# Optimization experiments

Measured on AMD Instinct MI355X. Metric: run time of the kernel, lower is better.

The kernel has to match this reference:

```python
import jax, jax.numpy as jnp
import numpy as np

N = 50000      # nodes
E = 100000     # edges
F_NODE = 128
F_EDGE = 16
H = 64         # hidden_dim
OUT = 32
STEPS = 3
G = 64         # num_graphs (static; batch.max()+1 in torch)


def setup_inputs() -> dict:
    key = jax.random.key(0)
    ks = jax.random.split(key, 20)

    def lin(k, fin, fout):
        s = 1.0 / np.sqrt(fin)
        return jax.random.uniform(k, (fin, fout), jnp.float32, -s, s)

    def bias(k, fin, fout):
        s = 1.0 / np.sqrt(fin)
        return jax.random.uniform(k, (fout,), jnp.float32, -s, s)

    inp = {
        'x': jax.random.normal(ks[0], (N, F_NODE), jnp.float32),
        'edge_index': jax.random.randint(ks[1], (2, E), 0, N),
        'edge_attr': jax.random.normal(ks[2], (E, F_EDGE), jnp.float32),
        'batch': jnp.sort(jax.random.randint(ks[3], (N,), 0, G)),
        # node encoder
        'W_enc': lin(ks[4], F_NODE, H), 'b_enc': bias(ks[5], F_NODE, H),
        # edge_nn: Linear(F_EDGE,H) -> ReLU -> Linear(H, H*H)
        'W_e1': lin(ks[6], F_EDGE, H), 'b_e1': bias(ks[7], F_EDGE, H),
        'W_e2': lin(ks[8], H, H * H), 'b_e2': bias(ks[9], H, H * H),
        # GRUCell (torch layout: [3H, H])
        'W_ih': jax.random.uniform(ks[10], (3 * H, H), jnp.float32, -1/np.sqrt(H), 1/np.sqrt(H)),
        'W_hh': jax.random.uniform(ks[11], (3 * H, H), jnp.float32, -1/np.sqrt(H), 1/np.sqrt(H)),
        'b_ih': jax.random.uniform(ks[12], (3 * H,), jnp.float32, -1/np.sqrt(H), 1/np.sqrt(H)),
        'b_hh': jax.random.uniform(ks[13], (3 * H,), jnp.float32, -1/np.sqrt(H), 1/np.sqrt(H)),
        # readout MLP: Linear(H,H) -> ReLU -> Linear(H,OUT)
        'W_r1': lin(ks[14], H, H), 'b_r1': bias(ks[15], H, H),
        'W_r2': lin(ks[16], H, OUT), 'b_r2': bias(ks[17], H, OUT),
    }
    return inp


def gru_cell(m, h, W_ih, W_hh, b_ih, b_hh):
    gi = m @ W_ih.T + b_ih   # [N, 3H]
    gh = h @ W_hh.T + b_hh
    i_r, i_z, i_n = jnp.split(gi, 3, axis=-1)
    h_r, h_z, h_n = jnp.split(gh, 3, axis=-1)
    r = jax.nn.sigmoid(i_r + h_r)
    z = jax.nn.sigmoid(i_z + h_z)
    n = jnp.tanh(i_n + r * h_n)
    return (1.0 - z) * n + z * h


def reference(x, edge_index, edge_attr, batch, W_enc, b_enc, W_e1, b_e1,
              W_e2, b_e2, W_ih, W_hh, b_ih, b_hh, W_r1, b_r1, W_r2, b_r2):
    h = x @ W_enc + b_enc                                   # [N, H]
    src, dst = edge_index[0], edge_index[1]
    # edge-conditioned weight matrices (loop-invariant; compute once)
    ew = (jax.nn.relu(edge_attr @ W_e1 + b_e1) @ W_e2 + b_e2).reshape(E, H, H)
    for _ in range(STEPS):
        msg = jnp.einsum('eij,ej->ei', ew, h[src])          # per-edge matvec
        m_agg = jax.ops.segment_sum(msg, dst, num_segments=N)
        h = gru_cell(m_agg, h, W_ih, W_hh, b_ih, b_hh)
    g = jax.ops.segment_sum(h, batch, num_segments=G)       # sum readout
    return jax.nn.relu(g @ W_r1 + b_r1) @ W_r2 + b_r2
```

## Files before the change

### kernel.cpp

```cpp
#include <hip/hip_runtime.h>
#include <hip/hip_bf16.h>
#include <math.h>

#define NN 50000
#define NE 100000
#define FN 128
#define FE 16
#define HD 64
#define OUTD 32
#define NG 64
#define ZK 65

typedef unsigned int uint;
typedef unsigned short ushort;
typedef __attribute__((ext_vector_type(8))) short short8;
typedef __attribute__((ext_vector_type(16))) float f32x16;

static __device__ __forceinline__ float bfbits2f(uint u) {
    return __builtin_bit_cast(float, u << 16);
}
static __device__ __forceinline__ uint packbf(float f0, float f1) {
    return __builtin_amdgcn_perm(__builtin_bit_cast(uint, f1),
                                 __builtin_bit_cast(uint, f0), 0x07060302u);
}
static __device__ __forceinline__ ushort f2bf(float f) {
    uint u = __builtin_bit_cast(uint, f);
    u = (u + 0x7FFFu + ((u >> 16) & 1u)) >> 16;
    return (ushort)u;
}
static __device__ __forceinline__ uint pack2rne(float f0, float f1) {
    return (uint)f2bf(f0) | ((uint)f2bf(f1) << 16);
}
static __device__ __forceinline__ float fsigmoid(float x) {
    return 1.f / (1.f + __expf(-x));
}
static __device__ __forceinline__ float ftanh(float x) {
    float t = __expf(2.f * x);
    return 1.f - 2.f / (t + 1.f);
}

#define PREP_S0 (ZK * 4096)
#define PREP_S1 (256 * 128)
__global__ void k_prep(const float* __restrict__ W_e2, const float* __restrict__ b_e2,
                       const float* __restrict__ W_ih, const float* __restrict__ W_hh,
                       ushort* __restrict__ Wtb, ushort* __restrict__ Bg) {
    int idx = blockIdx.x * 256 + threadIdx.x;
    if (idx < PREP_S0) {
        int k0 = idx >> 12, r = idx & 4095;
        int i = r >> 6, j = r & 63;
        float v = (k0 < 64) ? W_e2[k0 * 4096 + i * 64 + j] : b_e2[i * 64 + j];
        Wtb[idx] = f2bf(v);
        return;
    }
    idx -= PREP_S0;
    if (idx < PREP_S1) {
        int n = idx >> 7, k = idx & 127;
        int g = n >> 6, i = n & 63;
        float v = 0.f;
        if (g == 0)      v = (k < 64) ? W_ih[i * 64 + k]         : W_hh[i * 64 + (k - 64)];
        else if (g == 1) v = (k < 64) ? W_ih[(64 + i) * 64 + k]  : W_hh[(64 + i) * 64 + (k - 64)];
        else if (g == 2) v = (k < 64) ? W_ih[(128 + i) * 64 + k] : 0.f;
        else             v = (k < 64) ? 0.f                      : W_hh[(128 + i) * 64 + (k - 64)];
        Bg[idx] = f2bf(v);
    }
}

#define NBENC ((NN + 127) / 128)
#define NBEDG ((NE + 255) / 256)
__global__ __launch_bounds__(256, 2)
void k_enc_edge(const float* __restrict__ x, const float* __restrict__ W_enc,
                const float* __restrict__ b_enc,
                const float* __restrict__ ea, const float* __restrict__ W_e1,
                const float* __restrict__ b_e1,
                float* __restrict__ h, ushort* __restrict__ hb,
                ushort* __restrict__ zbT) {
    int t = threadIdx.x;
    if (blockIdx.x < NBENC) {
        __shared__ __align__(16) ushort blds[64 * 128];
        int wave = t >> 6, lane = t & 63, l31 = lane & 31, lhi = lane >> 5;
        for (int idx = t; idx < 1024; idx += 256) {
            int n = idx >> 4, p = idx & 15;
            int ssrc = p ^ (n & 15);
            int kk = ssrc * 8;
            uint4 u;
            u.x = pack2rne(W_enc[(kk + 0) * 64 + n], W_enc[(kk + 1) * 64 + n]);
            u.y = pack2rne(W_enc[(kk + 2) * 64 + n], W_enc[(kk + 3) * 64 + n]);
            u.z = pack2rne(W_enc[(kk + 4) * 64 + n], W_enc[(kk + 5) * 64 + n]);
            u.w = pack2rne(W_enc[(kk + 6) * 64 + n], W_enc[(kk + 7) * 64 + n]);
            *(uint4*)&blds[idx * 8] = u;
        }
        int node0 = blockIdx.x * 128 + wave * 32;
        int m = node0 + l31;
        int mc = (m < NN) ? m : NN - 1;
        short8 afr[8];
        const float* xr = x + (size_t)mc * 128;
        #pragma unroll
        for (int ks = 0; ks < 8; ks++) {
            float4 v0 = *(const float4*)(xr + ks * 16 + lhi * 8);
            float4 v1 = *(const float4*)(xr + ks * 16 + lhi * 8 + 4);
            uint4 u;
            u.x = pack2rne(v0.x, v0.y); u.y = pack2rne(v0.z, v0.w);
            u.z = pack2rne(v1.x, v1.y); u.w = pack2rne(v1.z, v1.w);
            afr[ks] = __builtin_bit_cast(short8, u);
        }
        __syncthreads();
        #pragma unroll
        for (int ct = 0; ct < 2; ct++) {
            f32x16 acc = {0};
            int n = ct * 32 + l31;
            #pragma unroll
            for (int ks = 0; ks < 8; ks++) {
                int sp = (ks * 2 + lhi) ^ (n & 15);
                short8 bf = *(const short8*)&blds[n * 128 + sp * 8];
                acc = __builtin_amdgcn_mfma_f32_32x32x16_bf16(afr[ks], bf, acc, 0, 0, 0);
            }
            int o = ct * 32 + l31;
            float bias = b_enc[o];
            #pragma unroll
            for (int r = 0; r < 16; r++) {
                int row = (r & 3) + 8 * (r >> 2) + 4 * lhi;
                int node = node0 + row;
                if (node < NN) {
                    float v = acc[r] + bias;
                    h[node * 64 + o] = v;
                    hb[node * 64 + o] = f2bf(v);
                }
            }
        }
    } else {
        __shared__ float Ws[16 * 64];
        __shared__ float b1s[64];
        for (int idx = t; idx < 1024; idx += 256) Ws[idx] = W_e1[idx];
        if (t < 64) b1s[t] = b_e1[t];
        __syncthreads();
        int e = (blockIdx.x - NBENC) * 256 + t;
        int ec = (e < NE) ? e : NE - 1;
        float eav[16];
        const float4* ep = (const float4*)(ea + ec * 16);
        #pragma unroll
        for (int q = 0; q < 4; q++) {
            float4 v = ep[q];
            eav[q * 4 + 0] = v.x; eav[q * 4 + 1] = v.y; eav[q * 4 + 2] = v.z; eav[q * 4 + 3] = v.w;
        }
        if (e >= NE) return;
        #pragma unroll 4
        for (int k = 0; k < 64; k++) {
            float acc = b1s[k];
            #pragma unroll
            for (int f = 0; f < 16; f++) acc += eav[f] * Ws[f * 64 + k];
            zbT[(size_t)k * NE + e] = f2bf(fmaxf(acc, 0.f));
        }
        zbT[(size_t)64 * NE + e] = f2bf(1.0f);
    }
}

__global__ __launch_bounds__(256, 2)
void k_message(const ushort* __restrict__ zbT, const ushort* __restrict__ hb,
               const int* __restrict__ eidx, const ushort* __restrict__ Wtb,
               float* __restrict__ m_agg) {
    __shared__ __align__(16) ushort wlds[2][2 * 4096];
    __shared__ __align__(16) ushort zlds[72 * 256];
    __shared__ int sdst[256];

    int t = threadIdx.x;
    int wave = t >> 6, lane = t & 63;
    int l31 = lane & 31, lhi = lane >> 5;
    int eblk = blockIdx.x * 256;
    int e0 = eblk + wave * 64;

    {
        int e = eblk + t; if (e >= NE) e = NE - 1;
        sdst[t] = eidx[NE + e];
    }

    float hf[2][32];
    #pragma unroll
    for (int mt = 0; mt < 2; mt++) {
        int e = e0 + mt * 32 + l31;
        int ec = (e < NE) ? e : NE - 1;
        int s = eidx[ec];
        const ushort* hrow = hb + (size_t)s * 64;
        #pragma unroll
        for (int c = 0; c < 4; c++) {
            uint4 v = *(const uint4*)(hrow + c * 16 + lhi * 8);
            hf[mt][c * 8 + 0] = bfbits2f(v.x & 0xFFFFu); hf[mt][c * 8 + 1] = bfbits2f(v.x >> 16);
            hf[mt][c * 8 + 2] = bfbits2f(v.y & 0xFFFFu); hf[mt][c * 8 + 3] = bfbits2f(v.y >> 16);
            hf[mt][c * 8 + 4] = bfbits2f(v.z & 0xFFFFu); hf[mt][c * 8 + 5] = bfbits2f(v.z >> 16);
            hf[mt][c * 8 + 6] = bfbits2f(v.w & 0xFFFFu); hf[mt][c * 8 + 7] = bfbits2f(v.w >> 16);
        }
    }

    #pragma unroll
    for (int call = 0; call < 9; call++) {
        int slot = call * 256 + t;
        int k0 = slot >> 5; if (k0 > 64) k0 = 64;
        int p = slot & 31;
        const ushort* src = zbT + (size_t)k0 * NE + eblk + p * 8;
        __builtin_amdgcn_global_load_lds(
            (const __attribute__((address_space(1))) void*)src,
            (__attribute__((address_space(3))) void*)&zlds[(size_t)(call * 256 + wave * 64) * 8],
            16, 0, 0);
    }

    auto stagew = [&](int slab0, int buf) {
        #pragma unroll
        for (int call = 0; call < 4; call++) {
            int slot = call * 256 + t;
            int slab = slab0 + (slot >> 9);
            if (slab > 64) slab = 64;
            int w = slot & 511;
            int i = w >> 3, jbp = w & 7;
            int jbg = jbp ^ (i & 7);
            const ushort* src = Wtb + (size_t)slab * 4096 + i * 64 + jbg * 8;
            __builtin_amdgcn_global_load_lds(
                (const __attribute__((address_space(1))) void*)src,
                (__attribute__((address_space(3))) void*)&wlds[buf][(size_t)(call * 256 + wave * 64) * 8],
                16, 0, 0);
        }
    };
    stagew(0, 0);

    f32x16 acc00 = {0}, acc01 = {0}, acc10 = {0}, acc11 = {0};

    for (int rnd = 0; rnd < 33; rnd++) {
        __syncthreads();
        int buf = rnd & 1;
        if (rnd < 32) stagew(2 * rnd + 2, buf ^ 1);
        int nk = (rnd < 32) ? 2 : 1;
        #pragma unroll 2
        for (int kk = 0; kk < nk; kk++) {
            int k0 = 2 * rnd + kk;
            float zf0 = bfbits2f((uint)zlds[k0 * 256 + wave * 64 + l31]);
            float zf1 = bfbits2f((uint)zlds[k0 * 256 + wave * 64 + 32 + l31]);
            const ushort* wb = &wlds[buf][kk * 4096];
            #pragma unroll
            for (int c = 0; c < 4; c++) {
                int jb = c * 2 + lhi;
                short8 b0 = *(const short8*)&wb[((0 * 32 + l31) << 6) + ((jb ^ (l31 & 7)) << 3)];
                short8 b1 = *(const short8*)&wb[((32 + l31) << 6) + ((jb ^ (l31 & 7)) << 3)];
                uint4 au0, au1;
                au0.x = packbf(zf0 * hf[0][c * 8 + 0], zf0 * hf[0][c * 8 + 1]);
                au0.y = packbf(zf0 * hf[0][c * 8 + 2], zf0 * hf[0][c * 8 + 3]);
                au0.z = packbf(zf0 * hf[0][c * 8 + 4], zf0 * hf[0][c * 8 + 5]);
                au0.w = packbf(zf0 * hf[0][c * 8 + 6], zf0 * hf[0][c * 8 + 7]);
                au1.x = packbf(zf1 * hf[1][c * 8 + 0], zf1 * hf[1][c * 8 + 1]);
                au1.y = packbf(zf1 * hf[1][c * 8 + 2], zf1 * hf[1][c * 8 + 3]);
                au1.z = packbf(zf1 * hf[1][c * 8 + 4], zf1 * hf[1][c * 8 + 5]);
                au1.w = packbf(zf1 * hf[1][c * 8 + 6], zf1 * hf[1][c * 8 + 7]);
                short8 a0 = __builtin_bit_cast(short8, au0);
                short8 a1 = __builtin_bit_cast(short8, au1);
                acc00 = __builtin_amdgcn_mfma_f32_32x32x16_bf16(a0, b0, acc00, 0, 0, 0);
                acc01 = __builtin_amdgcn_mfma_f32_32x32x16_bf16(a0, b1, acc01, 0, 0, 0);
                acc10 = __builtin_amdgcn_mfma_f32_32x32x16_bf16(a1, b0, acc10, 0, 0, 0);
                acc11 = __builtin_amdgcn_mfma_f32_32x32x16_bf16(a1, b1, acc11, 0, 0, 0);
            }
        }
    }

    #pragma unroll
    for (int r = 0; r < 16; r++) {
        int roff = (r & 3) + 8 * (r >> 2) + 4 * lhi;
        int eA = e0 + roff, eB = e0 + 32 + roff;
        if (eA < NE) {
            int d0 = sdst[wave * 64 + roff];
            atomicAdd(m_agg + d0 * 64 + l31,      acc00[r]);
            atomicAdd(m_agg + d0 * 64 + 32 + l31, acc01[r]);
        }
        if (eB < NE) {
            int d1 = sdst[wave * 64 + 32 + roff];
            atomicAdd(m_agg + d1 * 64 + l31,      acc10[r]);
            atomicAdd(m_agg + d1 * 64 + 32 + l31, acc11[r]);
        }
    }
}

__global__ __launch_bounds__(256, 2)
void k_gru(const float* __restrict__ magg, const float* __restrict__ h,
           const ushort* __restrict__ hb, const ushort* __restrict__ Bg,
           const float* __restrict__ b_ih, const float* __restrict__ b_hh,
           float* __restrict__ h_out, ushort* __restrict__ hb_out) {
    __shared__ __align__(16) ushort blds[256 * 128];
    int t = threadIdx.x;
    int wave = t >> 6, lane = t & 63, l31 = lane & 31, lhi = lane >> 5;
    for (int idx = t; idx < 4096; idx += 256) {
        int n = idx >> 4, p = idx & 15;
        int ssrc = p ^ (n & 15);
        *(uint4*)&blds[idx * 8] = *(const uint4*)&Bg[n * 128 + ssrc * 8];
    }
    int node0 = blockIdx.x * 128 + wave * 32;
    int m = node0 + l31;
    int mc = (m < NN) ? m : NN - 1;
    short8 afr[8];
    const float* mrow = magg + (size_t)mc * 64;
    #pragma unroll
    for (int ks = 0; ks < 4; ks++) {
        float4 v0 = *(const float4*)(mrow + ks * 16 + lhi * 8);
        float4 v1 = *(const float4*)(mrow + ks * 16 + lhi * 8 + 4);
        uint4 u;
        u.x = pack2rne(v0.x, v0.y); u.y = pack2rne(v0.z, v0.w);
        u.z = pack2rne(v1.x, v1.y); u.w = pack2rne(v1.z, v1.w);
        afr[ks] = __builtin_bit_cast(short8, u);
    }
    const ushort* hrow = hb + (size_t)mc * 64;
    #pragma unroll
    for (int ks = 4; ks < 8; ks++) {
        uint4 v = *(const uint4*)(hrow + (ks - 4) * 16 + lhi * 8);
        afr[ks] = __builtin_bit_cast(short8, v);
    }
    __syncthreads();
    #pragma unroll
    for (int ct = 0; ct < 2; ct++) {
        f32x16 aR = {0}, aZ = {0}, aI = {0}, aH = {0};
        int nR = 0   + ct * 32 + l31;
        int nZ = 64  + ct * 32 + l31;
        int nI = 128 + ct * 32 + l31;
        int nH = 192 + ct * 32 + l31;
        #pragma unroll
        for (int ks = 0; ks < 8; ks++) {
            int s = ks * 2 + lhi;
            short8 a = afr[ks];
            short8 bR = *(const short8*)&blds[nR * 128 + (s ^ (nR & 15)) * 8];
            short8 bZ = *(const short8*)&blds[nZ * 128 + (s ^ (nZ & 15)) * 8];
            short8 bI = *(const short8*)&blds[nI * 128 + (s ^ (nI & 15)) * 8];
            short8 bH = *(const short8*)&blds[nH * 128 + (s ^ (nH & 15)) * 8];
            aR = __builtin_amdgcn_mfma_f32_32x32x16_bf16(a, bR, aR, 0, 0, 0);
            aZ = __builtin_amdgcn_mfma_f32_32x32x16_bf16(a, bZ, aZ, 0, 0, 0);
            aI = __builtin_amdgcn_mfma_f32_32x32x16_bf16(a, bI, aI, 0, 0, 0);
            aH = __builtin_amdgcn_mfma_f32_32x32x16_bf16(a, bH, aH, 0, 0, 0);
        }
        int i = ct * 32 + l31;
        float brv = b_ih[i] + b_hh[i];
        float bzv = b_ih[64 + i] + b_hh[64 + i];
        float biv = b_ih[128 + i];
        float bhv = b_hh[128 + i];
        #pragma unroll
        for (int r = 0; r < 16; r++) {
            int row = (r & 3) + 8 * (r >> 2) + 4 * lhi;
            int node = node0 + row;
            if (node < NN) {
                float ho = h[node * 64 + i];
                float rg = fsigmoid(aR[r] + brv);
                float zg = fsigmoid(aZ[r] + bzv);
                float ng = ftanh(aI[r] + biv + rg * (aH[r] + bhv));
                float hv = (1.f - zg) * ng + zg * ho;
                h_out[node * 64 + i] = hv;
                hb_out[node * 64 + i] = f2bf(hv);
            }
        }
    }
}

__global__ __launch_bounds__(256)
void k_scatter_g(const float* __restrict__ h, const int* __restrict__ batch,
                 float* __restrict__ g) {
    int t = threadIdx.x;
    int i = t & 63, sub = t >> 6;
    int n0 = blockIdx.x * 64 + sub * 16;
    if (n0 >= NN) return;
    float acc = 0.f;
    int curg = batch[n0];
    for (int q = 0; q < 16; q++) {
        int n = n0 + q;
        if (n >= NN) break;
        int gq = batch[n];
        if (gq != curg) {
            atomicAdd(&g[curg * 64 + i], acc);
            acc = 0.f; curg = gq;
        }
        acc += h[n * 64 + i];
    }
    atomicAdd(&g[curg * 64 + i], acc);
}

__global__ __launch_bounds__(1024)
void k_readout(const float* __restrict__ g, const float* __restrict__ W1, const float* __restrict__ b1,
               const float* __restrict__ W2, const float* __restrict__ b2, float* __restrict__ out) {
    __shared__ float gs[64 * 64];
    __shared__ float ts[64 * 64];
    int t = threadIdx.x;
    for (int idx = t; idx < 4096; idx += 1024) gs[idx] = g[idx];
    __syncthreads();
    for (int idx = t; idx < 4096; idx += 1024) {
        int r = idx >> 6, c = idx & 63;
        float acc = b1[c];
        #pragma unroll 8
        for (int k = 0; k < 64; k++) acc += gs[r * 64 + k] * W1[k * 64 + c];
        ts[idx] = fmaxf(acc, 0.f);
    }
    __syncthreads();
    for (int idx = t; idx < 2048; idx += 1024) {
        int r = idx >> 5, c = idx & 31;
        float acc = b2[c];
        #pragma unroll 8
        for (int k = 0; k < 64; k++) acc += ts[r * 64 + k] * W2[k * 32 + c];
        out[idx] = acc;
    }
}

extern "C" void kernel_launch(void* const* d_in, const int* in_sizes, int n_in,
                              void* d_out, int out_size, void* d_ws, size_t ws_size,
                              hipStream_t stream) {
    const float* x     = (const float*)d_in[0];
    const int*   ei    = (const int*)  d_in[1];
    const float* ea    = (const float*)d_in[2];
    const int*   batch = (const int*)  d_in[3];
    const float* W_enc = (const float*)d_in[4];
    const float* b_enc = (const float*)d_in[5];
    const float* W_e1  = (const float*)d_in[6];
    const float* b_e1  = (const float*)d_in[7];
    const float* W_e2  = (const float*)d_in[8];
    const float* b_e2  = (const float*)d_in[9];
    const float* W_ih  = (const float*)d_in[10];
    const float* W_hh  = (const float*)d_in[11];
    const float* b_ih  = (const float*)d_in[12];
    const float* b_hh  = (const float*)d_in[13];
    const float* W_r1  = (const float*)d_in[14];
    const float* b_r1  = (const float*)d_in[15];
    const float* W_r2  = (const float*)d_in[16];
    const float* b_r2  = (const float*)d_in[17];
    float* out = (float*)d_out;

    float* ws    = (float*)d_ws;
    float* h     = ws;
    float* h2    = h    + NN * 64;
    float* magg  = h2   + NN * 64;
    float* g     = magg + NN * 64;
    ushort* hb   = (ushort*)(g + NG * 64);
    ushort* hb2  = hb   + NN * 64;
    ushort* zbT  = hb2  + NN * 64;
    ushort* Wtb  = zbT  + (size_t)ZK * NE;
    ushort* Bgru = Wtb  + ZK * 4096;

    hipLaunchKernelGGL(k_prep, dim3((PREP_S0 + PREP_S1 + 255) / 256), dim3(256), 0, stream,
                       W_e2, b_e2, W_ih, W_hh, Wtb, Bgru);
    hipLaunchKernelGGL(k_enc_edge, dim3(NBENC + NBEDG), dim3(256), 0, stream,
                       x, W_enc, b_enc, ea, W_e1, b_e1, h, hb, zbT);

    float* hc = h;    float* hn = h2;
    ushort* hbc = hb; ushort* hbn = hb2;
    for (int s = 0; s < 3; s++) {
        hipMemsetAsync(magg, 0, (size_t)NN * 64 * sizeof(float), stream);
        hipLaunchKernelGGL(k_message, dim3((NE + 255) / 256), dim3(256), 0, stream,
                           zbT, hbc, ei, Wtb, magg);
        hipLaunchKernelGGL(k_gru,     dim3((NN + 127) / 128), dim3(256), 0, stream,
                           magg, hc, hbc, Bgru, b_ih, b_hh, hn, hbn);
        float* tf = hc; hc = hn; hn = tf;
        ushort* tb = hbc; hbc = hbn; hbn = tb;
    }

    hipMemsetAsync(g, 0, (size_t)NG * 64 * sizeof(float), stream);
    hipLaunchKernelGGL(k_scatter_g, dim3((NN + 63) / 64), dim3(256), 0, stream, hc, batch, g);
    hipLaunchKernelGGL(k_readout,   dim3(1), dim3(1024), 0, stream, g, W_r1, b_r1, W_r2, b_r2, out);
}
```

Before: 447.8 us.

## Shrink message tile to 128 edges, relayout edge weights, fuse magg zeroing into GRU

Each message block now covers 128 edges instead of 256, one 32-edge M tile per wave. This halves the accumulator and h-fragment registers and raises the launch-bounds occupancy target to 3 blocks per CU. The per-slab edge weights are re-laid-out in k_prep so B-fragment LDS reads are contiguous instead of XOR-swizzled. The GRU kernel stages its weights with global_load_lds and zeroes m_agg after reading it, which removes two of the three per-step memsets. The trade-off is that each block reloads the full weight slabs for half as many edges, doubling weight traffic per edge, and the new LDS reads may hit bank conflicts.

```diff
diff --git a/kernel.cpp b/kernel.cpp
--- a/kernel.cpp
+++ b/kernel.cpp
@@ -47,7 +47,8 @@
     int idx = blockIdx.x * 256 + threadIdx.x;
     if (idx < PREP_S0) {
         int k0 = idx >> 12, r = idx & 4095;
-        int i = r >> 6, j = r & 63;
+        int jb = r >> 9, i = (r >> 3) & 63, q = r & 7;
+        int j = jb * 8 + q;
         float v = (k0 < 64) ? W_e2[k0 * 4096 + i * 64 + j] : b_e2[i * 64 + j];
         Wtb[idx] = f2bf(v);
         return;
@@ -154,47 +155,46 @@
     }
 }
 
-__global__ __launch_bounds__(256, 2)
+__global__ __launch_bounds__(256, 3)
 void k_message(const ushort* __restrict__ zbT, const ushort* __restrict__ hb,
                const int* __restrict__ eidx, const ushort* __restrict__ Wtb,
                float* __restrict__ m_agg) {
     __shared__ __align__(16) ushort wlds[2][2 * 4096];
-    __shared__ __align__(16) ushort zlds[72 * 256];
-    __shared__ int sdst[256];
+    __shared__ __align__(16) ushort zlds[1280 * 8];
+    __shared__ int sdst[128];
 
     int t = threadIdx.x;
     int wave = t >> 6, lane = t & 63;
     int l31 = lane & 31, lhi = lane >> 5;
-    int eblk = blockIdx.x * 256;
-    int e0 = eblk + wave * 64;
-
-    {
+    int eblk = blockIdx.x * 128;
+    int e0 = eblk + wave * 32;
+
+    if (t < 128) {
         int e = eblk + t; if (e >= NE) e = NE - 1;
         sdst[t] = eidx[NE + e];
     }
 
-    float hf[2][32];
-    #pragma unroll
-    for (int mt = 0; mt < 2; mt++) {
-        int e = e0 + mt * 32 + l31;
+    float hf[32];
+    {
+        int e = e0 + l31;
         int ec = (e < NE) ? e : NE - 1;
         int s = eidx[ec];
         const ushort* hrow = hb + (size_t)s * 64;
         #pragma unroll
         for (int c = 0; c < 4; c++) {
             uint4 v = *(const uint4*)(hrow + c * 16 + lhi * 8);
-            hf[mt][c * 8 + 0] = bfbits2f(v.x & 0xFFFFu); hf[mt][c * 8 + 1] = bfbits2f(v.x >> 16);
-            hf[mt][c * 8 + 2] = bfbits2f(v.y & 0xFFFFu); hf[mt][c * 8 + 3] = bfbits2f(v.y >> 16);
-            hf[mt][c * 8 + 4] = bfbits2f(v.z & 0xFFFFu); hf[mt][c * 8 + 5] = bfbits2f(v.z >> 16);
-            hf[mt][c * 8 + 6] = bfbits2f(v.w & 0xFFFFu); hf[mt][c * 8 + 7] = bfbits2f(v.w >> 16);
-        }
-    }
-
-    #pragma unroll
-    for (int call = 0; call < 9; call++) {
+            hf[c * 8 + 0] = bfbits2f(v.x & 0xFFFFu); hf[c * 8 + 1] = bfbits2f(v.x >> 16);
+            hf[c * 8 + 2] = bfbits2f(v.y & 0xFFFFu); hf[c * 8 + 3] = bfbits2f(v.y >> 16);
+            hf[c * 8 + 4] = bfbits2f(v.z & 0xFFFFu); hf[c * 8 + 5] = bfbits2f(v.z >> 16);
+            hf[c * 8 + 6] = bfbits2f(v.w & 0xFFFFu); hf[c * 8 + 7] = bfbits2f(v.w >> 16);
+        }
+    }
+
+    #pragma unroll
+    for (int call = 0; call < 5; call++) {
         int slot = call * 256 + t;
-        int k0 = slot >> 5; if (k0 > 64) k0 = 64;
-        int p = slot & 31;
+        int k0 = slot >> 4; if (k0 > 64) k0 = 64;
+        int p = slot & 15;
         const ushort* src = zbT + (size_t)k0 * NE + eblk + p * 8;
         __builtin_amdgcn_global_load_lds(
             (const __attribute__((address_space(1))) void*)src,
@@ -209,9 +209,7 @@
             int slab = slab0 + (slot >> 9);
             if (slab > 64) slab = 64;
             int w = slot & 511;
-            int i = w >> 3, jbp = w & 7;
-            int jbg = jbp ^ (i & 7);
-            const ushort* src = Wtb + (size_t)slab * 4096 + i * 64 + jbg * 8;
+            const ushort* src = Wtb + (size_t)slab * 4096 + w * 8;
             __builtin_amdgcn_global_load_lds(
                 (const __attribute__((address_space(1))) void*)src,
                 (__attribute__((address_space(3))) void*)&wlds[buf][(size_t)(call * 256 + wave * 64) * 8],
@@ -220,7 +218,7 @@
     };
     stagew(0, 0);
 
-    f32x16 acc00 = {0}, acc01 = {0}, acc10 = {0}, acc11 = {0};
+    f32x16 acc0 = {0}, acc1 = {0};
 
     for (int rnd = 0; rnd < 33; rnd++) {
         __syncthreads();
@@ -230,29 +228,21 @@
         #pragma unroll 2
         for (int kk = 0; kk < nk; kk++) {
             int k0 = 2 * rnd + kk;
-            float zf0 = bfbits2f((uint)zlds[k0 * 256 + wave * 64 + l31]);
-            float zf1 = bfbits2f((uint)zlds[k0 * 256 + wave * 64 + 32 + l31]);
+            float zf = bfbits2f((uint)zlds[k0 * 128 + wave * 32 + l31]);
             const ushort* wb = &wlds[buf][kk * 4096];
             #pragma unroll
             for (int c = 0; c < 4; c++) {
                 int jb = c * 2 + lhi;
-                short8 b0 = *(const short8*)&wb[((0 * 32 + l31) << 6) + ((jb ^ (l31 & 7)) << 3)];
-                short8 b1 = *(const short8*)&wb[((32 + l31) << 6) + ((jb ^ (l31 & 7)) << 3)];
-                uint4 au0, au1;
-                au0.x = packbf(zf0 * hf[0][c * 8 + 0], zf0 * hf[0][c * 8 + 1]);
-                au0.y = packbf(zf0 * hf[0][c * 8 + 2], zf0 * hf[0][c * 8 + 3]);
-                au0.z = packbf(zf0 * hf[0][c * 8 + 4], zf0 * hf[0][c * 8 + 5]);
-                au0.w = packbf(zf0 * hf[0][c * 8 + 6], zf0 * hf[0][c * 8 + 7]);
-                au1.x = packbf(zf1 * hf[1][c * 8 + 0], zf1 * hf[1][c * 8 + 1]);
-                au1.y = packbf(zf1 * hf[1][c * 8 + 2], zf1 * hf[1][c * 8 + 3]);
-                au1.z = packbf(zf1 * hf[1][c * 8 + 4], zf1 * hf[1][c * 8 + 5]);
-                au1.w = packbf(zf1 * hf[1][c * 8 + 6], zf1 * hf[1][c * 8 + 7]);
-                short8 a0 = __builtin_bit_cast(short8, au0);
-                short8 a1 = __builtin_bit_cast(short8, au1);
-                acc00 = __builtin_amdgcn_mfma_f32_32x32x16_bf16(a0, b0, acc00, 0, 0, 0);
-                acc01 = __builtin_amdgcn_mfma_f32_32x32x16_bf16(a0, b1, acc01, 0, 0, 0);
-                acc10 = __builtin_amdgcn_mfma_f32_32x32x16_bf16(a1, b0, acc10, 0, 0, 0);
-                acc11 = __builtin_amdgcn_mfma_f32_32x32x16_bf16(a1, b1, acc11, 0, 0, 0);
+                short8 b0 = *(const short8*)&wb[(jb * 64 + l31) * 8];
+                short8 b1 = *(const short8*)&wb[(jb * 64 + 32 + l31) * 8];
+                uint4 au;
+                au.x = packbf(zf * hf[c * 8 + 0], zf * hf[c * 8 + 1]);
+                au.y = packbf(zf * hf[c * 8 + 2], zf * hf[c * 8 + 3]);
+                au.z = packbf(zf * hf[c * 8 + 4], zf * hf[c * 8 + 5]);
+                au.w = packbf(zf * hf[c * 8 + 6], zf * hf[c * 8 + 7]);
+                short8 a = __builtin_bit_cast(short8, au);
+                acc0 = __builtin_amdgcn_mfma_f32_32x32x16_bf16(a, b0, acc0, 0, 0, 0);
+                acc1 = __builtin_amdgcn_mfma_f32_32x32x16_bf16(a, b1, acc1, 0, 0, 0);
             }
         }
     }
@@ -260,38 +250,39 @@
     #pragma unroll
     for (int r = 0; r < 16; r++) {
         int roff = (r & 3) + 8 * (r >> 2) + 4 * lhi;
-        int eA = e0 + roff, eB = e0 + 32 + roff;
-        if (eA < NE) {
-            int d0 = sdst[wave * 64 + roff];
-            atomicAdd(m_agg + d0 * 64 + l31,      acc00[r]);
-            atomicAdd(m_agg + d0 * 64 + 32 + l31, acc01[r]);
-        }
-        if (eB < NE) {
-            int d1 = sdst[wave * 64 + 32 + roff];
-            atomicAdd(m_agg + d1 * 64 + l31,      acc10[r]);
-            atomicAdd(m_agg + d1 * 64 + 32 + l31, acc11[r]);
+        int e = e0 + roff;
+        if (e < NE) {
+            int d = sdst[wave * 32 + roff];
+            atomicAdd(m_agg + d * 64 + l31,      acc0[r]);
+            atomicAdd(m_agg + d * 64 + 32 + l31, acc1[r]);
         }
     }
 }
 
 __global__ __launch_bounds__(256, 2)
-void k_gru(const float* __restrict__ magg, const float* __restrict__ h,
+void k_gru(float* __restrict__ magg, const float* __restrict__ h,
            const ushort* __restrict__ hb, const ushort* __restrict__ Bg,
            const float* __restrict__ b_ih, const float* __restrict__ b_hh,
            float* __restrict__ h_out, ushort* __restrict__ hb_out) {
     __shared__ __align__(16) ushort blds[256 * 128];
     int t = threadIdx.x;
     int wave = t >> 6, lane = t & 63, l31 = lane & 31, lhi = lane >> 5;
-    for (int idx = t; idx < 4096; idx += 256) {
-        int n = idx >> 4, p = idx & 15;
+    #pragma unroll
+    for (int call = 0; call < 16; call++) {
+        int slot = call * 256 + t;
+        int n = slot >> 4, p = slot & 15;
         int ssrc = p ^ (n & 15);
-        *(uint4*)&blds[idx * 8] = *(const uint4*)&Bg[n * 128 + ssrc * 8];
+        const ushort* src = Bg + n * 128 + ssrc * 8;
+        __builtin_amdgcn_global_load_lds(
+            (const __attribute__((address_space(1))) void*)src,
+            (__attribute__((address_space(3))) void*)&blds[(size_t)(call * 256 + wave * 64) * 8],
+            16, 0, 0);
     }
     int node0 = blockIdx.x * 128 + wave * 32;
     int m = node0 + l31;
     int mc = (m < NN) ? m : NN - 1;
     short8 afr[8];
-    const float* mrow = magg + (size_t)mc * 64;
+    float* mrow = magg + (size_t)mc * 64;
     #pragma unroll
     for (int ks = 0; ks < 4; ks++) {
         float4 v0 = *(const float4*)(mrow + ks * 16 + lhi * 8);
@@ -300,6 +291,12 @@
         u.x = pack2rne(v0.x, v0.y); u.y = pack2rne(v0.z, v0.w);
         u.z = pack2rne(v1.x, v1.y); u.w = pack2rne(v1.z, v1.w);
         afr[ks] = __builtin_bit_cast(short8, u);
+    }
+    float4 z4 = make_float4(0.f, 0.f, 0.f, 0.f);
+    #pragma unroll
+    for (int ks = 0; ks < 4; ks++) {
+        *(float4*)(mrow + ks * 16 + lhi * 8) = z4;
+        *(float4*)(mrow + ks * 16 + lhi * 8 + 4) = z4;
     }
     const ushort* hrow = hb + (size_t)mc * 64;
     #pragma unroll
@@ -435,12 +432,12 @@
                        W_e2, b_e2, W_ih, W_hh, Wtb, Bgru);
     hipLaunchKernelGGL(k_enc_edge, dim3(NBENC + NBEDG), dim3(256), 0, stream,
                        x, W_enc, b_enc, ea, W_e1, b_e1, h, hb, zbT);
+    hipMemsetAsync(magg, 0, (size_t)NN * 64 * sizeof(float), stream);
 
     float* hc = h;    float* hn = h2;
     ushort* hbc = hb; ushort* hbn = hb2;
     for (int s = 0; s < 3; s++) {
-        hipMemsetAsync(magg, 0, (size_t)NN * 64 * sizeof(float), stream);
-        hipLaunchKernelGGL(k_message, dim3((NE + 255) / 256), dim3(256), 0, stream,
+        hipLaunchKernelGGL(k_message, dim3((NE + 127) / 128), dim3(256), 0, stream,
                            zbT, hbc, ei, Wtb, magg);
         hipLaunchKernelGGL(k_gru,     dim3((NN + 127) / 128), dim3(256), 0, stream,
                            magg, hc, hbc, Bgru, b_ih, b_hh, hn, hbn);
```

Measured after the change: 453.4 us. No clear change (+1.2%).

## Drop fp32 hidden state, fuse magg zeroing and graph readout into GRU kernel

Applied to the files above, without the earlier changes.

The fp32 copy of the hidden state is removed. The GRU now reads the previous h from its bf16 copy, which lowers precision in the z*h term. The GRU kernel zeroes m_agg after reading it, replacing the per-step memsets. On the final step it atomically adds into the graph sums, replacing the separate scatter kernel and its memset. The W_e2 slab layout is changed to a jb-major order so the message kernel can stage with plain contiguous loads, and the GRU weight staging now uses direct global-to-LDS loads. Together these cut memory traffic and kernel launches, at the cost of many more atomics on the final step and some accumulated rounding error.

```diff
diff --git a/kernel.cpp b/kernel.cpp
--- a/kernel.cpp
+++ b/kernel.cpp
@@ -47,7 +47,8 @@
     int idx = blockIdx.x * 256 + threadIdx.x;
     if (idx < PREP_S0) {
         int k0 = idx >> 12, r = idx & 4095;
-        int i = r >> 6, j = r & 63;
+        int jb = r >> 9, i = (r >> 3) & 63, q = r & 7;
+        int j = jb * 8 + q;
         float v = (k0 < 64) ? W_e2[k0 * 4096 + i * 64 + j] : b_e2[i * 64 + j];
         Wtb[idx] = f2bf(v);
         return;
@@ -72,8 +73,7 @@
                 const float* __restrict__ b_enc,
                 const float* __restrict__ ea, const float* __restrict__ W_e1,
                 const float* __restrict__ b_e1,
-                float* __restrict__ h, ushort* __restrict__ hb,
-                ushort* __restrict__ zbT) {
+                ushort* __restrict__ hb, ushort* __restrict__ zbT) {
     int t = threadIdx.x;
     if (blockIdx.x < NBENC) {
         __shared__ __align__(16) ushort blds[64 * 128];
@@ -120,11 +120,7 @@
             for (int r = 0; r < 16; r++) {
                 int row = (r & 3) + 8 * (r >> 2) + 4 * lhi;
                 int node = node0 + row;
-                if (node < NN) {
-                    float v = acc[r] + bias;
-                    h[node * 64 + o] = v;
-                    hb[node * 64 + o] = f2bf(v);
-                }
+                if (node < NN) hb[node * 64 + o] = f2bf(acc[r] + bias);
             }
         }
     } else {
@@ -159,7 +155,7 @@
                const int* __restrict__ eidx, const ushort* __restrict__ Wtb,
                float* __restrict__ m_agg) {
     __shared__ __align__(16) ushort wlds[2][2 * 4096];
-    __shared__ __align__(16) ushort zlds[72 * 256];
+    __shared__ __align__(16) ushort zlds[2304 * 8];
     __shared__ int sdst[256];
 
     int t = threadIdx.x;
@@ -209,9 +205,7 @@
             int slab = slab0 + (slot >> 9);
             if (slab > 64) slab = 64;
             int w = slot & 511;
-            int i = w >> 3, jbp = w & 7;
-            int jbg = jbp ^ (i & 7);
-            const ushort* src = Wtb + (size_t)slab * 4096 + i * 64 + jbg * 8;
+            const ushort* src = Wtb + (size_t)slab * 4096 + w * 8;
             __builtin_amdgcn_global_load_lds(
                 (const __attribute__((address_space(1))) void*)src,
                 (__attribute__((address_space(3))) void*)&wlds[buf][(size_t)(call * 256 + wave * 64) * 8],
@@ -236,8 +230,8 @@
             #pragma unroll
             for (int c = 0; c < 4; c++) {
                 int jb = c * 2 + lhi;
-                short8 b0 = *(const short8*)&wb[((0 * 32 + l31) << 6) + ((jb ^ (l31 & 7)) << 3)];
-                short8 b1 = *(const short8*)&wb[((32 + l31) << 6) + ((jb ^ (l31 & 7)) << 3)];
+                short8 b0 = *(const short8*)&wb[(jb * 64 + l31) * 8];
+                short8 b1 = *(const short8*)&wb[(jb * 64 + 32 + l31) * 8];
                 uint4 au0, au1;
                 au0.x = packbf(zf0 * hf[0][c * 8 + 0], zf0 * hf[0][c * 8 + 1]);
                 au0.y = packbf(zf0 * hf[0][c * 8 + 2], zf0 * hf[0][c * 8 + 3]);
@@ -275,23 +269,29 @@
 }
 
 __global__ __launch_bounds__(256, 2)
-void k_gru(const float* __restrict__ magg, const float* __restrict__ h,
-           const ushort* __restrict__ hb, const ushort* __restrict__ Bg,
-           const float* __restrict__ b_ih, const float* __restrict__ b_hh,
-           float* __restrict__ h_out, ushort* __restrict__ hb_out) {
+void k_gru(float* __restrict__ magg, const ushort* __restrict__ hb,
+           const ushort* __restrict__ Bg, const float* __restrict__ b_ih,
+           const float* __restrict__ b_hh, ushort* __restrict__ hb_out,
+           const int* __restrict__ batch, float* __restrict__ g, int last) {
     __shared__ __align__(16) ushort blds[256 * 128];
     int t = threadIdx.x;
     int wave = t >> 6, lane = t & 63, l31 = lane & 31, lhi = lane >> 5;
-    for (int idx = t; idx < 4096; idx += 256) {
-        int n = idx >> 4, p = idx & 15;
+    #pragma unroll
+    for (int call = 0; call < 16; call++) {
+        int slot = call * 256 + t;
+        int n = slot >> 4, p = slot & 15;
         int ssrc = p ^ (n & 15);
-        *(uint4*)&blds[idx * 8] = *(const uint4*)&Bg[n * 128 + ssrc * 8];
+        const ushort* src = Bg + n * 128 + ssrc * 8;
+        __builtin_amdgcn_global_load_lds(
+            (const __attribute__((address_space(1))) void*)src,
+            (__attribute__((address_space(3))) void*)&blds[(size_t)(call * 256 + wave * 64) * 8],
+            16, 0, 0);
     }
     int node0 = blockIdx.x * 128 + wave * 32;
     int m = node0 + l31;
     int mc = (m < NN) ? m : NN - 1;
     short8 afr[8];
-    const float* mrow = magg + (size_t)mc * 64;
+    float* mrow = magg + (size_t)mc * 64;
     #pragma unroll
     for (int ks = 0; ks < 4; ks++) {
         float4 v0 = *(const float4*)(mrow + ks * 16 + lhi * 8);
@@ -300,6 +300,14 @@
         u.x = pack2rne(v0.x, v0.y); u.y = pack2rne(v0.z, v0.w);
         u.z = pack2rne(v1.x, v1.y); u.w = pack2rne(v1.z, v1.w);
         afr[ks] = __builtin_bit_cast(short8, u);
+    }
+    if (!last) {
+        float4 z4 = make_float4(0.f, 0.f, 0.f, 0.f);
+        #pragma unroll
+        for (int ks = 0; ks < 4; ks++) {
+            *(float4*)(mrow + ks * 16 + lhi * 8) = z4;
+            *(float4*)(mrow + ks * 16 + lhi * 8 + 4) = z4;
+        }
     }
     const ushort* hrow = hb + (size_t)mc * 64;
     #pragma unroll
@@ -338,38 +346,16 @@
             int row = (r & 3) + 8 * (r >> 2) + 4 * lhi;
             int node = node0 + row;
             if (node < NN) {
-                float ho = h[node * 64 + i];
+                float ho = bfbits2f((uint)hb[node * 64 + i]);
                 float rg = fsigmoid(aR[r] + brv);
                 float zg = fsigmoid(aZ[r] + bzv);
                 float ng = ftanh(aI[r] + biv + rg * (aH[r] + bhv));
                 float hv = (1.f - zg) * ng + zg * ho;
-                h_out[node * 64 + i] = hv;
-                hb_out[node * 64 + i] = f2bf(hv);
+                if (!last) hb_out[node * 64 + i] = f2bf(hv);
+                else       atomicAdd(&g[batch[node] * 64 + i], hv);
             }
         }
     }
-}
-
-__global__ __launch_bounds__(256)
-void k_scatter_g(const float* __restrict__ h, const int* __restrict__ batch,
-                 float* __restrict__ g) {
-    int t = threadIdx.x;
-    int i = t & 63, sub = t >> 6;
-    int n0 = blockIdx.x * 64 + sub * 16;
-    if (n0 >= NN) return;
-    float acc = 0.f;
-    int curg = batch[n0];
-    for (int q = 0; q < 16; q++) {
-        int n = n0 + q;
-        if (n >= NN) break;
-        int gq = batch[n];
-        if (gq != curg) {
-            atomicAdd(&g[curg * 64 + i], acc);
-            acc = 0.f; curg = gq;
-        }
-        acc += h[n * 64 + i];
-    }
-    atomicAdd(&g[curg * 64 + i], acc);
 }
 
 __global__ __launch_bounds__(1024)
@@ -421,9 +407,7 @@
     float* out = (float*)d_out;
 
     float* ws    = (float*)d_ws;
-    float* h     = ws;
-    float* h2    = h    + NN * 64;
-    float* magg  = h2   + NN * 64;
+    float* magg  = ws;
     float* g     = magg + NN * 64;
     ushort* hb   = (ushort*)(g + NG * 64);
     ushort* hb2  = hb   + NN * 64;
@@ -434,21 +418,18 @@
     hipLaunchKernelGGL(k_prep, dim3((PREP_S0 + PREP_S1 + 255) / 256), dim3(256), 0, stream,
                        W_e2, b_e2, W_ih, W_hh, Wtb, Bgru);
     hipLaunchKernelGGL(k_enc_edge, dim3(NBENC + NBEDG), dim3(256), 0, stream,
-                       x, W_enc, b_enc, ea, W_e1, b_e1, h, hb, zbT);
-
-    float* hc = h;    float* hn = h2;
+                       x, W_enc, b_enc, ea, W_e1, b_e1, hb, zbT);
+    hipMemsetAsync(magg, 0, (size_t)NN * 64 * sizeof(float), stream);
+    hipMemsetAsync(g, 0, (size_t)NG * 64 * sizeof(float), stream);
+
     ushort* hbc = hb; ushort* hbn = hb2;
     for (int s = 0; s < 3; s++) {
-        hipMemsetAsync(magg, 0, (size_t)NN * 64 * sizeof(float), stream);
         hipLaunchKernelGGL(k_message, dim3((NE + 255) / 256), dim3(256), 0, stream,
                            zbT, hbc, ei, Wtb, magg);
         hipLaunchKernelGGL(k_gru,     dim3((NN + 127) / 128), dim3(256), 0, stream,
-                           magg, hc, hbc, Bgru, b_ih, b_hh, hn, hbn);
-        float* tf = hc; hc = hn; hn = tf;
+                           magg, hbc, Bgru, b_ih, b_hh, hbn, batch, g, (s == 2) ? 1 : 0);
         ushort* tb = hbc; hbc = hbn; hbn = tb;
     }
 
-    hipMemsetAsync(g, 0, (size_t)NG * 64 * sizeof(float), stream);
-    hipLaunchKernelGGL(k_scatter_g, dim3((NN + 63) / 64), dim3(256), 0, stream, hc, batch, g);
-    hipLaunchKernelGGL(k_readout,   dim3(1), dim3(1024), 0, stream, g, W_r1, b_r1, W_r2, b_r2, out);
-}
+    hipLaunchKernelGGL(k_readout, dim3(1), dim3(1024), 0, stream, g, W_r1, b_r1, W_r2, b_r2, out);
+}
```

New measurement: 451.0 us. No clear change (+0.7%).
